# Kernel optimization log

Measured on AMD Instinct MI355X. Metric: run time of the kernel, lower is better.

Reference implementation:

```python
import jax, jax.numpy as jnp
import numpy as np

EMBED_DIM = 1024
N_HEADS = 16
HEAD_DIM = EMBED_DIM // N_HEADS


def setup_inputs() -> dict:
    key = jax.random.key(0)
    ks = jax.random.split(key, 8)
    B, Tq, Tk, C = 2, 2048, 2048, EMBED_DIM
    s = 1.0 / np.sqrt(C)
    return {
        "query": jax.random.normal(ks[0], (B, Tq, C), jnp.float32),
        "context": jax.random.normal(ks[1], (B, Tk, C), jnp.float32),
        "Wq": jax.random.normal(ks[2], (C, C), jnp.float32) * s,
        "bq": jnp.zeros((C,), jnp.float32),
        "Wkv": jax.random.normal(ks[3], (C, 2 * C), jnp.float32) * s,
        "bkv": jnp.zeros((2 * C,), jnp.float32),
        "Wo": jax.random.normal(ks[4], (C, C), jnp.float32) * s,
        "bo": jnp.zeros((C,), jnp.float32),
    }


def reference(query, context, Wq, bq, Wkv, bkv, Wo, bo):
    B, Tq, C = query.shape
    Tk = context.shape[1]
    H, D = N_HEADS, HEAD_DIM
    # projections
    q = (query @ Wq + bq).reshape(B, Tq, H, D)        # [B,Tq,H,D]
    kv = (context @ Wkv + bkv).reshape(B, Tk, 2, H, D)
    k = kv[:, :, 0]                                   # [B,Tk,H,D]
    v = kv[:, :, 1]
    scale = D ** -0.5
    # attention scores [B,H,Tq,Tk]
    attn = jnp.einsum("bqhd,bkhd->bhqk", q, k) * scale
    attn = jax.nn.softmax(attn, axis=-1)
    # dropout p=0.0 -> identity in eval / p=0
    out = jnp.einsum("bhqk,bkhd->bqhd", attn, v).reshape(B, Tq, C)
    return out @ Wo + bo
```

## Files before the change

### kernel.cpp

```cpp
#include <hip/hip_runtime.h>
#include <math.h>

typedef unsigned short u16;
typedef unsigned int u32;
typedef __attribute__((ext_vector_type(8))) short short8;
typedef __attribute__((ext_vector_type(4))) short short4v;
typedef __attribute__((ext_vector_type(4))) float f32x4;

__device__ __forceinline__ u16 f2bf(float f) {
  union { float f; unsigned u; } x; x.f = f;
  unsigned r = x.u + 0x7FFFu + ((x.u >> 16) & 1u);
  return (u16)(r >> 16);
}

__device__ __forceinline__ u32 asu(float f) {
  union { float f; u32 u; } x; x.f = f; return x.u;
}

__device__ __forceinline__ u32 pack2bf(float a, float b) {
  return __builtin_amdgcn_perm(asu(b) + 0x8000u, asu(a) + 0x8000u, 0x07060302u);
}

__device__ __forceinline__ u32 cvtpk2bf(float a, float b) {
  u32 r;
  asm("v_cvt_pk_bf16_f32 %0, %1, %2" : "=v"(r) : "v"(a), "v"(b));
  return r;
}

__device__ __forceinline__ void gld_lds16(const void* g, void* l) {
  __builtin_amdgcn_global_load_lds(
      (const __attribute__((address_space(1))) unsigned int*)g,
      (__attribute__((address_space(3))) unsigned int*)l, 16, 0, 0);
}

__global__ void pre_kernel(const float* __restrict__ q, const float* __restrict__ c,
                           const float* __restrict__ Wq, const float* __restrict__ Wkv,
                           const float* __restrict__ Wo,
                           u16* __restrict__ xq, u16* __restrict__ xc,
                           u16* __restrict__ WqF, u16* __restrict__ WkvF,
                           u16* __restrict__ WoF) {
  __shared__ float tile[32][33];
  int bx = blockIdx.x;
  int t = threadIdx.y * 32 + threadIdx.x;
  if (bx < 8192) {
    int i = bx * 256 + t;
    const float* src = q; u16* dst = xq;
    if (i >= 1048576) { i -= 1048576; src = c; dst = xc; }
    float4 v = ((const float4*)src)[i];
    ((uint2*)dst)[i] = make_uint2(
        (unsigned)f2bf(v.x) | ((unsigned)f2bf(v.y) << 16),
        (unsigned)f2bf(v.z) | ((unsigned)f2bf(v.w) << 16));
  } else {
    int g = bx - 8192;
    int gx = g & 127, gy = g >> 7;
    const float* src; u16* dst; int N, n0;
    if (gx < 32)      { src = Wq;  dst = WqF;  N = 1024; n0 = gx * 32; }
    else if (gx < 96) { src = Wkv; dst = WkvF; N = 2048; n0 = (gx - 32) * 32; }
    else              { src = Wo;  dst = WoF;  N = 1024; n0 = (gx - 96) * 32; }
    int k0 = gy * 32;
    int tx = threadIdx.x, ty = threadIdx.y;
#pragma unroll
    for (int i = 0; i < 4; ++i)
      tile[ty * 4 + i][tx] = src[(size_t)(k0 + ty * 4 + i) * N + n0 + tx];
    __syncthreads();
    int e = t * 4;
    int ch = e >> 9, rem = e & 511;
    int kg = (rem >> 7) & 3;
    int nl = (rem >> 3) & 15;
    int j0 = rem & 7;
    int kk = kg * 8 + j0;
    int nn = ch * 16 + nl;
    u32 lo = pack2bf(tile[kk][nn], tile[kk + 1][nn]);
    u32 hi = pack2bf(tile[kk + 2][nn], tile[kk + 3][nn]);
    *(uint2*)(dst + (size_t)(((n0 >> 4) + ch) * 32 + gy) * 512 + rem) = make_uint2(lo, hi);
  }
}

__global__ __launch_bounds__(256, 3) void qkv_gemm(
    const u16* __restrict__ Xq, const u16* __restrict__ Xc,
    const u16* __restrict__ WqF, const u16* __restrict__ WkvF,
    const float* __restrict__ bq, const float* __restrict__ bkv,
    u16* __restrict__ qb, u16* __restrict__ kf, u16* __restrict__ vf,
    float qscale) {
  __shared__ __align__(16) u16 smem[16896];
  const int tid = threadIdx.x, lane = tid & 63, wave = tid >> 6;
  const int quad = lane >> 4, cl = lane & 15;
  const int wr = (wave >> 1) * 64, wc = (wave & 1) * 64;

  const int xcd = blockIdx.x & 7, pos = blockIdx.x >> 3;
  const u16 *A, *Bf; const float* bias; int m0, n0; bool isq;
  if (pos < 64) {
    isq = false; A = Xc; Bf = WkvF; bias = bkv;
    m0 = ((xcd >> 1) * 8 + (pos >> 3)) * 128;
    n0 = ((xcd & 1) * 8 + (pos & 7)) * 128;
  } else {
    int p = pos - 64;
    isq = true;  A = Xq; Bf = WqF;  bias = bq;
    m0 = (xcd * 4 + (p >> 3)) * 128;
    n0 = (p & 7) * 128;
  }
  const int bn4 = (n0 + wc) >> 4;

  const int rA = lane >> 3;
  const int kcs = ((lane & 7) ^ rA) * 8;
  const int r7 = cl & 7;

  auto stageA = [&](int k0, int buf) {
    u16* As = smem + buf * 8192;
#pragma unroll
    for (int it = 0; it < 4; ++it) {
      int chunk = it * 4 + wave;
      gld_lds16(A + (size_t)(m0 + chunk * 8 + rA) * 1024 + k0 + kcs, As + chunk * 512);
    }
  };

  f32x4 acc[4][4] = {};
  short8 bA[2][4], bB[2][4];

  auto loadB = [&](short8 (&dst)[2][4], int k05) {
#pragma unroll
    for (int ks = 0; ks < 2; ++ks)
#pragma unroll
      for (int ni = 0; ni < 4; ++ni)
        dst[ks][ni] = *(const short8*)(Bf + (size_t)((bn4 + ni) * 32 + k05 + ks) * 512 + lane * 8);
  };

  auto compute = [&](const u16* As, short8 (&breg)[2][4]) {
#pragma unroll
    for (int ks = 0; ks < 2; ++ks) {
      short8 af[4];
#pragma unroll
      for (int mi = 0; mi < 4; ++mi) {
        int row = wr + mi * 16 + cl;
        af[mi] = *(const short8*)(As + (row >> 3) * 512 + r7 * 64 +
                                  (((ks << 2) | quad) ^ r7) * 8);
      }
#pragma unroll
      for (int mi = 0; mi < 4; ++mi)
#pragma unroll
        for (int ni = 0; ni < 4; ++ni)
          acc[mi][ni] = __builtin_amdgcn_mfma_f32_16x16x32_bf16(af[mi], breg[ks][ni], acc[mi][ni], 0, 0, 0);
    }
  };

  stageA(0, 0);
  loadB(bA, 0);
  __syncthreads();

#pragma unroll 1
  for (int ii = 0; ii < 8; ++ii) {
    const int i = ii * 2;
    stageA((i + 1) * 64, 1);
    loadB(bB, (i + 1) * 2);
    compute(smem, bA);
    __syncthreads();
    const int j = i + 1;
    if (j < 15) { stageA((j + 1) * 64, 0); loadB(bA, (j + 1) * 2); }
    compute(smem + 8192, bB);
    __syncthreads();
  }

  if (isq) {
#pragma unroll
    for (int mi = 0; mi < 4; ++mi)
#pragma unroll
      for (int ni = 0; ni < 4; ++ni)
#pragma unroll
        for (int r = 0; r < 4; ++r) {
          int row = m0 + wr + mi * 16 + quad * 4 + r;
          int col = n0 + wc + ni * 16 + cl;
          qb[(size_t)row * 1024 + col] = f2bf((acc[mi][ni][r] + bias[col]) * qscale);
        }
    return;
  }

  const int b = m0 >> 11, kt0 = (m0 & 2047) >> 6;
  const bool kreg = (n0 < 1024);
  if (kreg) {
#pragma unroll
    for (int mi = 0; mi < 4; ++mi)
#pragma unroll
      for (int ni = 0; ni < 4; ++ni)
#pragma unroll
        for (int r = 0; r < 4; ++r)
          smem[(wr + mi * 16 + quad * 4 + r) * 132 + wc + ni * 16 + cl] =
              f2bf(acc[mi][ni][r] + bias[n0 + wc + ni * 16 + cl]);
    __syncthreads();
#pragma unroll
    for (int i = 0; i < 8; ++i) {
      int c = i * 4 + wave;
      int hs = c >> 4, ts = (c >> 3) & 1, ks = (c >> 2) & 1, idx = c & 3;
      int h = (n0 >> 6) + hs;
      size_t bhkt = ((size_t)((b * 16 + h) * 32 + kt0 + ts)) * 4096;
      short8 v = *(const short8*)(smem + (ts * 64 + idx * 16 + cl) * 132 +
                                  hs * 64 + ks * 32 + quad * 8);
      *(short8*)(kf + bhkt + (size_t)(ks * 4 + idx) * 512 + lane * 8) = v;
    }
  } else {
#pragma unroll
    for (int mi = 0; mi < 4; ++mi)
#pragma unroll
      for (int ni = 0; ni < 4; ++ni) {
        float v0 = acc[mi][ni][0] + bias[n0 + wc + ni * 16 + cl];
        float v1 = acc[mi][ni][1] + bias[n0 + wc + ni * 16 + cl];
        float v2 = acc[mi][ni][2] + bias[n0 + wc + ni * 16 + cl];
        float v3 = acc[mi][ni][3] + bias[n0 + wc + ni * 16 + cl];
        *(uint2*)(smem + (wc + ni * 16 + cl) * 132 + wr + mi * 16 + quad * 4) =
            make_uint2(pack2bf(v0, v1), pack2bf(v2, v3));
      }
    __syncthreads();
#pragma unroll
    for (int i = 0; i < 8; ++i) {
      int c = i * 4 + wave;
      int hs = c >> 4, ts = (c >> 3) & 1, ks = (c >> 2) & 1, idx = c & 3;
      int h = ((n0 - 1024) >> 6) + hs;
      size_t bhkt = ((size_t)((b * 16 + h) * 32 + kt0 + ts)) * 4096;
      const u16* src = smem + (hs * 64 + idx * 16 + cl) * 132 + ts * 64 + ks * 32 + quad * 4;
      short8 v;
      *(short4v*)&v       = *(const short4v*)(src);
      *((short4v*)&v + 1) = *(const short4v*)(src + 16);
      *(short8*)(vf + bhkt + (size_t)(ks * 4 + idx) * 512 + lane * 8) = v;
    }
  }
}

__global__ __launch_bounds__(256) void o_gemm(
    const u16* __restrict__ A, const u16* __restrict__ Bf,
    const float* __restrict__ bias, float* __restrict__ Cm) {
  __shared__ __align__(16) u16 smem[24576];
  const int tid = threadIdx.x, lane = tid & 63, wave = tid >> 6;
  const int quad = lane >> 4, cl = lane & 15;
  const int xcd = blockIdx.x & 7, pos = blockIdx.x >> 3;
  const int m0 = (xcd * 8 + (pos >> 3)) * 64, n0 = (pos & 7) * 128;
  const int wr = (wave >> 1) * 32, wc = (wave & 1) * 64;
  const int n04 = n0 >> 4;

  const int rA = lane >> 3;
  const int kcs = ((lane & 7) ^ rA) * 8;
  const int r7 = cl & 7;

  auto stageA = [&](int k0, int buf) {
    u16* As = smem + buf * 4096;
#pragma unroll
    for (int it = 0; it < 2; ++it) {
      int chunk = wave * 2 + it;
      gld_lds16(A + (size_t)(m0 + chunk * 8 + rA) * 1024 + k0 + kcs, As + chunk * 512);
    }
  };
  auto stageB = [&](int k0, int buf) {
    u16* Bs = smem + 8192 + buf * 8192;
    const int k05 = k0 >> 5;
#pragma unroll
    for (int it = 0; it < 4; ++it) {
      int c = it * 4 + wave;
      int j = c >> 1, ks = c & 1;
      gld_lds16(Bf + (size_t)((n04 + j) * 32 + k05 + ks) * 512 + lane * 8, Bs + c * 512);
    }
  };

  f32x4 acc[2][4] = {};

  stageA(0, 0);
  stageB(0, 0);
  __syncthreads();

  for (int i = 0; i < 16; ++i) {
    const int k0 = i * 64;
    const int cur = i & 1;
    if (i < 15) { stageA(k0 + 64, cur ^ 1); stageB(k0 + 64, cur ^ 1); }
    const u16* As = smem + cur * 4096;
    const u16* Bs = smem + 8192 + cur * 8192;
    short8 bf[2][4];
#pragma unroll
    for (int ks = 0; ks < 2; ++ks)
#pragma unroll
      for (int ni = 0; ni < 4; ++ni)
        bf[ks][ni] = *(const short8*)(Bs + (size_t)((((wave & 1) * 4 + ni) * 2 + ks) * 512) + lane * 8);
#pragma unroll
    for (int ks = 0; ks < 2; ++ks) {
      short8 af[2];
#pragma unroll
      for (int mi = 0; mi < 2; ++mi) {
        int row = wr + mi * 16 + cl;
        af[mi] = *(const short8*)(As + (row >> 3) * 512 + r7 * 64 +
                                  (((ks << 2) | quad) ^ r7) * 8);
      }
#pragma unroll
      for (int mi = 0; mi < 2; ++mi)
#pragma unroll
        for (int ni = 0; ni < 4; ++ni)
          acc[mi][ni] = __builtin_amdgcn_mfma_f32_16x16x32_bf16(af[mi], bf[ks][ni], acc[mi][ni], 0, 0, 0);
    }
    __syncthreads();
  }
#pragma unroll
  for (int mi = 0; mi < 2; ++mi)
#pragma unroll
    for (int ni = 0; ni < 4; ++ni)
#pragma unroll
      for (int r = 0; r < 4; ++r) {
        int row = m0 + wr + mi * 16 + quad * 4 + r;
        int col = n0 + wc + ni * 16 + cl;
        Cm[(size_t)row * 1024 + col] = acc[mi][ni][r] + bias[col];
      }
}

__global__ __launch_bounds__(512, 4) void flash_attn(
    const u16* __restrict__ qb, const u16* __restrict__ kf,
    const u16* __restrict__ vf, u16* __restrict__ outp) {
  __shared__ __align__(16) u16 kv[2][16 * 512];
  const int tid = threadIdx.x, lane = tid & 63, wave = tid >> 6;
  const int quad = lane >> 4, cl = lane & 15;
  const int id = blockIdx.x;
  const int h = (id & 7) | (((id >> 3) & 1) << 3);
  const int b = (id >> 4) & 1;
  const int qt = id >> 5;

  const int qrow0 = b * 2048 + qt * 128 + wave * 16;
  short8 bq[2];
#pragma unroll
  for (int ks = 0; ks < 2; ++ks)
    bq[ks] = *(const short8*)(qb + (size_t)(qrow0 + cl) * 1024 + h * 64 + ks * 32 + quad * 8);

  short8 ones;
#pragma unroll
  for (int j = 0; j < 8; ++j) ones[j] = (short)0x3F80;

  const u16* kfb = kf + (size_t)((b * 16 + h) * 32) * 4096;
  const u16* vfb = vf + (size_t)((b * 16 + h) * 32) * 4096;

  auto stage = [&](int kt, int buf) {
#pragma unroll
    for (int i = 0; i < 2; ++i) {
      int c = wave * 2 + i;
      const u16* src = (c < 8) ? (kfb + (size_t)kt * 4096 + c * 512)
                               : (vfb + (size_t)kt * 4096 + (c - 8) * 512);
      gld_lds16(src + lane * 8, &kv[buf][c * 512]);
    }
  };

  f32x4 o_acc[4] = {};
  f32x4 l_acc = {};

  stage(0, 0);
  __syncthreads();

#pragma unroll 1
  for (int kt = 0; kt < 32; ++kt) {
    const int cur = kt & 1, nxt = cur ^ 1;
    if (kt < 31) stage(kt + 1, nxt);
    const u16* kb = &kv[cur][0];
    const u16* vb = &kv[cur][8 * 512];
    f32x4 st[4] = {};
    __builtin_amdgcn_s_setprio(1);
#pragma unroll
    for (int ks = 0; ks < 2; ++ks)
#pragma unroll
      for (int ni = 0; ni < 4; ++ni) {
        short8 ak = *(const short8*)(kb + (ks * 4 + ni) * 512 + lane * 8);
        st[ni] = __builtin_amdgcn_mfma_f32_16x16x32_bf16(ak, bq[ks], st[ni], 0, 0, 0);
      }
    __builtin_amdgcn_s_setprio(0);
    short8 av[2][4];
#pragma unroll
    for (int ks = 0; ks < 2; ++ks)
#pragma unroll
      for (int nd = 0; nd < 4; ++nd)
        av[ks][nd] = *(const short8*)(vb + (ks * 4 + nd) * 512 + lane * 8);
    u32 bp[2][4];
#pragma unroll
    for (int ni = 0; ni < 4; ++ni) {
      float p0 = __builtin_amdgcn_exp2f(st[ni][0]);
      float p1 = __builtin_amdgcn_exp2f(st[ni][1]);
      float p2 = __builtin_amdgcn_exp2f(st[ni][2]);
      float p3 = __builtin_amdgcn_exp2f(st[ni][3]);
      bp[ni >> 1][(ni & 1) * 2 + 0] = cvtpk2bf(p0, p1);
      bp[ni >> 1][(ni & 1) * 2 + 1] = cvtpk2bf(p2, p3);
    }
    __builtin_amdgcn_s_setprio(1);
#pragma unroll
    for (int ks = 0; ks < 2; ++ks) {
      short8 pb;
      *(u32*)&pb     = bp[ks][0];
      ((u32*)&pb)[1] = bp[ks][1];
      ((u32*)&pb)[2] = bp[ks][2];
      ((u32*)&pb)[3] = bp[ks][3];
#pragma unroll
      for (int nd = 0; nd < 4; ++nd)
        o_acc[nd] = __builtin_amdgcn_mfma_f32_16x16x32_bf16(av[ks][nd], pb, o_acc[nd], 0, 0, 0);
      l_acc = __builtin_amdgcn_mfma_f32_16x16x32_bf16(ones, pb, l_acc, 0, 0, 0);
    }
    __builtin_amdgcn_s_setprio(0);
    __syncthreads();
  }
  float inv = 1.f / l_acc[0];
  u16* Ow = &kv[0][wave * 16 * 68];
#pragma unroll
  for (int nd = 0; nd < 4; ++nd)
#pragma unroll
    for (int r2 = 0; r2 < 2; ++r2)
      *(u32*)(Ow + cl * 68 + nd * 16 + quad * 4 + r2 * 2) =
          cvtpk2bf(o_acc[nd][r2 * 2] * inv, o_acc[nd][r2 * 2 + 1] * inv);
#pragma unroll
  for (int half = 0; half < 2; ++half) {
    int row = half * 8 + (lane >> 3);
    int d0 = (lane & 7) * 8;
    short8 ov = *(const short8*)(Ow + row * 68 + d0);
    *(short8*)(outp + (size_t)(qrow0 + row) * 1024 + h * 64 + d0) = ov;
  }
}

extern "C" void kernel_launch(void* const* d_in, const int* in_sizes, int n_in,
                              void* d_out, int out_size, void* d_ws, size_t ws_size,
                              hipStream_t stream) {
  const float* query   = (const float*)d_in[0];
  const float* context = (const float*)d_in[1];
  const float* Wq  = (const float*)d_in[2];
  const float* bq  = (const float*)d_in[3];
  const float* Wkv = (const float*)d_in[4];
  const float* bkv = (const float*)d_in[5];
  const float* Wo  = (const float*)d_in[6];
  const float* bo  = (const float*)d_in[7];
  float* out = (float*)d_out;

  char* ws = (char*)d_ws;
  size_t off = 0;
  auto alloc = [&](size_t bytes) {
    char* p = ws + off;
    off += (bytes + 255) & ~(size_t)255;
    return p;
  };
  u16* buf0 = (u16*)alloc(4096ull * 1024 * 2);
  u16* xcb  = (u16*)alloc(4096ull * 1024 * 2);
  u16* WqF  = (u16*)alloc(1024ull * 1024 * 2);
  u16* WkvF = (u16*)alloc(2048ull * 1024 * 2);
  u16* WoF  = (u16*)alloc(1024ull * 1024 * 2);
  u16* qb   = (u16*)alloc(4096ull * 1024 * 2);
  u16* kfr  = (u16*)alloc(4ull * 1024 * 1024 * 2);
  u16* vfr  = (u16*)alloc(4ull * 1024 * 1024 * 2);

  const float QSCALE = 0.125f * 1.44269504f;

  pre_kernel<<<12288, dim3(32, 8), 0, stream>>>(query, context, Wq, Wkv, Wo,
                                                buf0, xcb, WqF, WkvF, WoF);
  qkv_gemm<<<768, 256, 0, stream>>>(buf0, xcb, WqF, WkvF, bq, bkv,
                                    qb, kfr, vfr, QSCALE);
  flash_attn<<<512, 512, 0, stream>>>(qb, kfr, vfr, buf0);
  o_gemm<<<512, 256, 0, stream>>>(buf0, WoF, bo, out);
}
```

Measured before the change: 182.7 us.

## Process two 16-row query tiles per wave in flash attention, halve block threads

Each wave now handles 32 query rows (two 16-row sub-tiles) rather than 16, so every K and V fragment read from LDS is reused by two MFMA chains. The block drops from 8 to 4 waves, and each wave stages four chunks per tile. The goal is less LDS read traffic per MFMA and more independent MFMA work to hide latency. The cost is roughly doubled accumulator and score registers and fewer waves per block, which could lower occupancy.

```diff
diff --git a/kernel.cpp b/kernel.cpp
--- a/kernel.cpp
+++ b/kernel.cpp
@@ -305,7 +305,7 @@
       }
 }
 
-__global__ __launch_bounds__(512, 4) void flash_attn(
+__global__ __launch_bounds__(256, 2) void flash_attn(
     const u16* __restrict__ qb, const u16* __restrict__ kf,
     const u16* __restrict__ vf, u16* __restrict__ outp) {
   __shared__ __align__(16) u16 kv[2][16 * 512];
@@ -316,11 +316,13 @@
   const int b = (id >> 4) & 1;
   const int qt = id >> 5;
 
-  const int qrow0 = b * 2048 + qt * 128 + wave * 16;
-  short8 bq[2];
-#pragma unroll
-  for (int ks = 0; ks < 2; ++ks)
-    bq[ks] = *(const short8*)(qb + (size_t)(qrow0 + cl) * 1024 + h * 64 + ks * 32 + quad * 8);
+  const int qrow0 = b * 2048 + qt * 128 + wave * 32;
+  short8 bq0[2], bq1[2];
+#pragma unroll
+  for (int ks = 0; ks < 2; ++ks) {
+    bq0[ks] = *(const short8*)(qb + (size_t)(qrow0 + cl) * 1024 + h * 64 + ks * 32 + quad * 8);
+    bq1[ks] = *(const short8*)(qb + (size_t)(qrow0 + 16 + cl) * 1024 + h * 64 + ks * 32 + quad * 8);
+  }
 
   short8 ones;
 #pragma unroll
@@ -331,34 +333,35 @@
 
   auto stage = [&](int kt, int buf) {
 #pragma unroll
-    for (int i = 0; i < 2; ++i) {
-      int c = wave * 2 + i;
+    for (int i = 0; i < 4; ++i) {
+      int c = wave * 4 + i;
       const u16* src = (c < 8) ? (kfb + (size_t)kt * 4096 + c * 512)
                                : (vfb + (size_t)kt * 4096 + (c - 8) * 512);
       gld_lds16(src + lane * 8, &kv[buf][c * 512]);
     }
   };
 
-  f32x4 o_acc[4] = {};
-  f32x4 l_acc = {};
+  f32x4 o0[4] = {}, o1[4] = {};
+  f32x4 l0 = {}, l1 = {};
 
   stage(0, 0);
   __syncthreads();
 
 #pragma unroll 1
   for (int kt = 0; kt < 32; ++kt) {
-    const int cur = kt & 1, nxt = cur ^ 1;
-    if (kt < 31) stage(kt + 1, nxt);
+    const int cur = kt & 1;
+    if (kt < 31) stage(kt + 1, cur ^ 1);
     const u16* kb = &kv[cur][0];
     const u16* vb = &kv[cur][8 * 512];
-    f32x4 st[4] = {};
+    f32x4 s0[4] = {}, s1[4] = {};
     __builtin_amdgcn_s_setprio(1);
 #pragma unroll
     for (int ks = 0; ks < 2; ++ks)
 #pragma unroll
       for (int ni = 0; ni < 4; ++ni) {
         short8 ak = *(const short8*)(kb + (ks * 4 + ni) * 512 + lane * 8);
-        st[ni] = __builtin_amdgcn_mfma_f32_16x16x32_bf16(ak, bq[ks], st[ni], 0, 0, 0);
+        s0[ni] = __builtin_amdgcn_mfma_f32_16x16x32_bf16(ak, bq0[ks], s0[ni], 0, 0, 0);
+        s1[ni] = __builtin_amdgcn_mfma_f32_16x16x32_bf16(ak, bq1[ks], s1[ni], 0, 0, 0);
       }
     __builtin_amdgcn_s_setprio(0);
     short8 av[2][4];
@@ -367,43 +370,59 @@
 #pragma unroll
       for (int nd = 0; nd < 4; ++nd)
         av[ks][nd] = *(const short8*)(vb + (ks * 4 + nd) * 512 + lane * 8);
-    u32 bp[2][4];
+    u32 bp0[2][4], bp1[2][4];
 #pragma unroll
     for (int ni = 0; ni < 4; ++ni) {
-      float p0 = __builtin_amdgcn_exp2f(st[ni][0]);
-      float p1 = __builtin_amdgcn_exp2f(st[ni][1]);
-      float p2 = __builtin_amdgcn_exp2f(st[ni][2]);
-      float p3 = __builtin_amdgcn_exp2f(st[ni][3]);
-      bp[ni >> 1][(ni & 1) * 2 + 0] = cvtpk2bf(p0, p1);
-      bp[ni >> 1][(ni & 1) * 2 + 1] = cvtpk2bf(p2, p3);
+      float a0 = __builtin_amdgcn_exp2f(s0[ni][0]);
+      float a1 = __builtin_amdgcn_exp2f(s0[ni][1]);
+      float a2 = __builtin_amdgcn_exp2f(s0[ni][2]);
+      float a3 = __builtin_amdgcn_exp2f(s0[ni][3]);
+      bp0[ni >> 1][(ni & 1) * 2 + 0] = cvtpk2bf(a0, a1);
+      bp0[ni >> 1][(ni & 1) * 2 + 1] = cvtpk2bf(a2, a3);
+      float c0 = __builtin_amdgcn_exp2f(s1[ni][0]);
+      float c1 = __builtin_amdgcn_exp2f(s1[ni][1]);
+      float c2 = __builtin_amdgcn_exp2f(s1[ni][2]);
+      float c3 = __builtin_amdgcn_exp2f(s1[ni][3]);
+      bp1[ni >> 1][(ni & 1) * 2 + 0] = cvtpk2bf(c0, c1);
+      bp1[ni >> 1][(ni & 1) * 2 + 1] = cvtpk2bf(c2, c3);
     }
     __builtin_amdgcn_s_setprio(1);
 #pragma unroll
     for (int ks = 0; ks < 2; ++ks) {
-      short8 pb;
-      *(u32*)&pb     = bp[ks][0];
-      ((u32*)&pb)[1] = bp[ks][1];
-      ((u32*)&pb)[2] = bp[ks][2];
-      ((u32*)&pb)[3] = bp[ks][3];
-#pragma unroll
-      for (int nd = 0; nd < 4; ++nd)
-        o_acc[nd] = __builtin_amdgcn_mfma_f32_16x16x32_bf16(av[ks][nd], pb, o_acc[nd], 0, 0, 0);
-      l_acc = __builtin_amdgcn_mfma_f32_16x16x32_bf16(ones, pb, l_acc, 0, 0, 0);
+      short8 pb0, pb1;
+      *(u32*)&pb0     = bp0[ks][0];
+      ((u32*)&pb0)[1] = bp0[ks][1];
+      ((u32*)&pb0)[2] = bp0[ks][2];
+      ((u32*)&pb0)[3] = bp0[ks][3];
+      *(u32*)&pb1     = bp1[ks][0];
+      ((u32*)&pb1)[1] = bp1[ks][1];
+      ((u32*)&pb1)[2] = bp1[ks][2];
+      ((u32*)&pb1)[3] = bp1[ks][3];
+#pragma unroll
+      for (int nd = 0; nd < 4; ++nd) {
+        o0[nd] = __builtin_amdgcn_mfma_f32_16x16x32_bf16(av[ks][nd], pb0, o0[nd], 0, 0, 0);
+        o1[nd] = __builtin_amdgcn_mfma_f32_16x16x32_bf16(av[ks][nd], pb1, o1[nd], 0, 0, 0);
+      }
+      l0 = __builtin_amdgcn_mfma_f32_16x16x32_bf16(ones, pb0, l0, 0, 0, 0);
+      l1 = __builtin_amdgcn_mfma_f32_16x16x32_bf16(ones, pb1, l1, 0, 0, 0);
     }
     __builtin_amdgcn_s_setprio(0);
     __syncthreads();
   }
-  float inv = 1.f / l_acc[0];
-  u16* Ow = &kv[0][wave * 16 * 68];
+  float inv0 = 1.f / l0[0], inv1 = 1.f / l1[0];
+  u16* Ow = &kv[0][wave * 32 * 68];
 #pragma unroll
   for (int nd = 0; nd < 4; ++nd)
 #pragma unroll
-    for (int r2 = 0; r2 < 2; ++r2)
+    for (int r2 = 0; r2 < 2; ++r2) {
       *(u32*)(Ow + cl * 68 + nd * 16 + quad * 4 + r2 * 2) =
-          cvtpk2bf(o_acc[nd][r2 * 2] * inv, o_acc[nd][r2 * 2 + 1] * inv);
-#pragma unroll
-  for (int half = 0; half < 2; ++half) {
-    int row = half * 8 + (lane >> 3);
+          cvtpk2bf(o0[nd][r2 * 2] * inv0, o0[nd][r2 * 2 + 1] * inv0);
+      *(u32*)(Ow + (16 + cl) * 68 + nd * 16 + quad * 4 + r2 * 2) =
+          cvtpk2bf(o1[nd][r2 * 2] * inv1, o1[nd][r2 * 2 + 1] * inv1);
+    }
+#pragma unroll
+  for (int p = 0; p < 4; ++p) {
+    int row = p * 8 + (lane >> 3);
     int d0 = (lane & 7) * 8;
     short8 ov = *(const short8*)(Ow + row * 68 + d0);
     *(short8*)(outp + (size_t)(qrow0 + row) * 1024 + h * 64 + d0) = ov;
@@ -445,6 +464,6 @@
                                                 buf0, xcb, WqF, WkvF, WoF);
   qkv_gemm<<<768, 256, 0, stream>>>(buf0, xcb, WqF, WkvF, bq, bkv,
                                     qb, kfr, vfr, QSCALE);
-  flash_attn<<<512, 512, 0, stream>>>(qb, kfr, vfr, buf0);
+  flash_attn<<<512, 256, 0, stream>>>(qb, kfr, vfr, buf0);
   o_gemm<<<512, 256, 0, stream>>>(buf0, WoF, bo, out);
 }
```

Result: no change. 182.3 us (median of 3 runs) (-0.2%).
